# Performance work log

Hardware: AMD Instinct MI355X
Metric: run time of the kernel (lower is better)

The kernel has to match this reference:

```python
import jax, jax.numpy as jnp
import numpy as np

IN, H, B, T = 64, 256, 128, 512

def _uniform(key, shape, std):
    return jax.random.uniform(key, shape, jnp.float32, -std, std)

def setup_inputs() -> dict:
    key = jax.random.key(0)
    ks = jax.random.split(key, 16)
    std = 1.0 / np.sqrt(H)
    inp = {
        'x': jax.random.normal(ks[0], (B, T, IN), jnp.float32),
        # layer 1 sLSTM cell
        'Wxh1': _uniform(ks[1], (4 * H, IN), std), 'bxh1': _uniform(ks[2], (4 * H,), std),
        'Whh1': _uniform(ks[3], (4 * H, H), std),  'bhh1': _uniform(ks[4], (4 * H,), std),
        # layer 2 sLSTM cell
        'Wxh2': _uniform(ks[5], (4 * H, H), std),  'bxh2': _uniform(ks[6], (4 * H,), std),
        'Whh2': _uniform(ks[7], (4 * H, H), std),  'bhh2': _uniform(ks[8], (4 * H,), std),
        # head MLP
        'W1': _uniform(ks[9], (H // 2, H), 1.0 / np.sqrt(H)),      'b1': _uniform(ks[10], (H // 2,), 1.0 / np.sqrt(H)),
        'W2': _uniform(ks[11], (H // 4, H // 2), 1.0 / np.sqrt(H // 2)), 'b2': _uniform(ks[12], (H // 4,), 1.0 / np.sqrt(H // 2)),
        'W3': _uniform(ks[13], (1, H // 4), 1.0 / np.sqrt(H // 4)),      'b3': _uniform(ks[14], (1,), 1.0 / np.sqrt(H // 4)),
    }
    return inp

def _slstm_cell(x, h, c, m, n, Wxh, bxh, Whh, bhh):
    # gates: [B, 4H]
    gates = x @ Wxh.T + bxh + h @ Whh.T + bhh
    ig, fg, zg, og = jnp.split(gates, 4, axis=1)
    z_t = jnp.tanh(zg)
    o_t = jax.nn.sigmoid(og)
    # stabilizer: log(exp(fg)) = fg, log(exp(ig)) = ig
    m_t = jnp.maximum(fg + m, ig)
    i_t = jnp.exp(ig - m_t)
    f_t = jnp.exp(fg + m - m_t)
    c_t = f_t * c + i_t * z_t
    n_t = f_t * n + i_t
    h_t = o_t * (c_t / n_t)
    return h_t, c_t, m_t, n_t

def reference(x, Wxh1, bxh1, Whh1, bhh1, Wxh2, bxh2, Whh2, bhh2, W1, b1, W2, b2, W3, b3):
    Bq = x.shape[0]
    z = jnp.zeros((Bq, H), x.dtype)
    init = (z, z, z, z, z, z, z, z)  # (h1,c1,m1,n1,h2,c2,m2,n2)

    def step(carry, x_t):
        h1, c1, m1, n1, h2, c2, m2, n2 = carry
        h1, c1, m1, n1 = _slstm_cell(x_t, h1, c1, m1, n1, Wxh1, bxh1, Whh1, bhh1)
        h2, c2, m2, n2 = _slstm_cell(h1, h2, c2, m2, n2, Wxh2, bxh2, Whh2, bhh2)
        return (h1, c1, m1, n1, h2, c2, m2, n2), None

    carry, _ = jax.lax.scan(step, init, jnp.swapaxes(x, 0, 1))  # scan over time
    out = carry[4]  # last h2 == outputs[:, -1, :]
    out = jax.nn.relu(out @ W1.T + b1)   # dropout is identity in eval
    out = jax.nn.relu(out @ W2.T + b2)
    out = out @ W3.T + b3
    return out.squeeze(-1)  # [B]
```

## Files before the change

### kernel.cpp

```cpp
#include <hip/hip_runtime.h>
#include <stdint.h>

typedef unsigned short ushort_t;
typedef __attribute__((ext_vector_type(8))) short short8;
typedef __attribute__((ext_vector_type(4))) float float4v;
typedef __attribute__((ext_vector_type(4))) int int4v;

#define TSTEPS 512
#define NBATCH 128
#define HID 256
#define NIN 64
#define RB 32
#define NBHID (NBATCH*HID)
#define RING_DW (RB*NBHID)

#define OFF_FLAGS   0u
#define OFF_BIAS    16384u
#define OFF_H1R     32768u
#define RING_BYTES  (RB*(unsigned)NBATCH*HID*4u)
#define OFF_H2R     (OFF_H1R + RING_BYTES)
#define OFF_WF1     (OFF_H2R + RING_BYTES)
#define WF1_FRAGS   (16*8*4*4)
#define OFF_WF2     (OFF_WF1 + WF1_FRAGS*1024u)
#define WF2_FRAGS   (16*8*6*4)
#define OFF_HOUT    (OFF_WF2 + WF2_FRAGS*1024u)


__device__ __forceinline__ ushort_t bf16h(float f) {
    unsigned u = __float_as_uint(f);
    u += 0x7fffu + ((u >> 16) & 1u);
    return (ushort_t)(u >> 16);
}
__device__ __forceinline__ float bf16f(ushort_t h) {
    return __uint_as_float(((unsigned)h) << 16);
}
__device__ __forceinline__ unsigned genbit(int s) {
    return ((unsigned)(s + 64) >> 5) & 1u;
}


__device__ __forceinline__ int ld_cg_i32(const void* p) {
    int r;
    asm volatile("global_load_dword %0, %1, off sc0 sc1\n\ts_waitcnt vmcnt(0)"
                 : "=v"(r) : "v"(p) : "memory");
    return r;
}
__device__ __forceinline__ float ld_cg_f32(const void* p) {
    float r;
    asm volatile("global_load_dword %0, %1, off sc0 sc1\n\ts_waitcnt vmcnt(0)"
                 : "=v"(r) : "v"(p) : "memory");
    return r;
}
__device__ __forceinline__ void ld2x4(int4v& a, int4v& b, const void* p) {
    asm volatile("global_load_dwordx4 %0, %2, off sc0 sc1\n\t"
                 "global_load_dwordx4 %1, %2, off offset:16 sc0 sc1\n\t"
                 "s_waitcnt vmcnt(0)"
                 : "=&v"(a), "=&v"(b) : "v"(p) : "memory");
}
__device__ __forceinline__ void ld4x4(int4v& a, int4v& b, int4v& c, int4v& d,
                                      const void* p, const void* q) {
    asm volatile("global_load_dwordx4 %0, %4, off sc0 sc1\n\t"
                 "global_load_dwordx4 %1, %4, off offset:16 sc0 sc1\n\t"
                 "global_load_dwordx4 %2, %5, off sc0 sc1\n\t"
                 "global_load_dwordx4 %3, %5, off offset:16 sc0 sc1\n\t"
                 "s_waitcnt vmcnt(0)"
                 : "=&v"(a), "=&v"(b), "=&v"(c), "=&v"(d)
                 : "v"(p), "v"(q) : "memory");
}
__device__ __forceinline__ void st_cg_u32(void* p, unsigned v) {
    asm volatile("global_store_dword %0, %1, off sc0 sc1" :: "v"(p), "v"(v) : "memory");
}
__device__ __forceinline__ void st_cg_i32(int* p, int v) {
    asm volatile("global_store_dword %0, %1, off sc0 sc1" :: "v"(p), "v"(v) : "memory");
}
__device__ __forceinline__ void st_cg_f32(void* p, float v) {
    asm volatile("global_store_dword %0, %1, off sc0 sc1" :: "v"(p), "v"(v) : "memory");
}

__device__ __forceinline__ bool tag8(int4v a, int4v b, unsigned gw) {
    unsigned x = ((unsigned)a[0] ^ gw) | ((unsigned)a[1] ^ gw) |
                 ((unsigned)a[2] ^ gw) | ((unsigned)a[3] ^ gw) |
                 ((unsigned)b[0] ^ gw) | ((unsigned)b[1] ^ gw) |
                 ((unsigned)b[2] ^ gw) | ((unsigned)b[3] ^ gw);
    return (x & 1u) == 0u;
}

__device__ __forceinline__ int4v ext_hi8(int4v a, int4v b) {
    int4v r;
    r[0] = (int)__builtin_amdgcn_perm((unsigned)a[1], (unsigned)a[0], 0x05040100u);
    r[1] = (int)__builtin_amdgcn_perm((unsigned)a[3], (unsigned)a[2], 0x05040100u);
    r[2] = (int)__builtin_amdgcn_perm((unsigned)b[1], (unsigned)b[0], 0x05040100u);
    r[3] = (int)__builtin_amdgcn_perm((unsigned)b[3], (unsigned)b[2], 0x05040100u);
    return r;
}
__device__ __forceinline__ int4v ext_lo8(int4v a, int4v b) {
    int4v r;
    r[0] = (int)__builtin_amdgcn_perm((unsigned)a[1], (unsigned)a[0], 0x07060302u);
    r[1] = (int)__builtin_amdgcn_perm((unsigned)a[3], (unsigned)a[2], 0x07060302u);
    r[2] = (int)__builtin_amdgcn_perm((unsigned)b[1], (unsigned)b[0], 0x07060302u);
    r[3] = (int)__builtin_amdgcn_perm((unsigned)b[3], (unsigned)b[2], 0x07060302u);
    return r;
}


__global__ void prep_misc(const float* bxh1, const float* bhh1,
                          const float* bxh2, const float* bhh2,
                          float* bias, int* flags, unsigned* ring_all)
{
    int n = blockIdx.x * blockDim.x + threadIdx.x;
    if (n < 1024)       bias[n] = bxh1[n] + bhh1[n];
    else if (n < 2048)  bias[n] = bxh2[n - 1024] + bhh2[n - 1024];
    else if (n < 6144)  flags[n - 2048] = 0;
    else {
        unsigned d = n - 6144;
        if (d < 2u * RING_DW)
            ring_all[d] = 0x00000001u;
    }
}

__global__ void prep_wf(const float* Wxh1, const float* Whh1,
                        const float* Wxh2, const float* Whh2,
                        ushort_t* wf1, ushort_t* wf2)
{
    int n = blockIdx.x * blockDim.x + threadIdx.x;
    const int L1E = WF1_FRAGS * 512;
    const int L2E = WF2_FRAGS * 512;
    if (n >= L1E + L2E) return;
    int layer = (n >= L1E) ? 1 : 0;
    int e = layer ? (n - L1E) : n;
    int el = e & 511;
    int f  = e >> 9;
    int lane = el >> 3, j = el & 7;
    int nt = f & 3;
    int rem = f >> 2;
    int i, wv, slice, F, S;
    if (!layer) { F = 4; S = 10; i = rem & 3; wv = (rem >> 2) & 7; slice = rem >> 5; }
    else        { F = 6; S = 16; i = rem % 6; int r2 = rem / 6; wv = r2 & 7; slice = r2 >> 3; }
    int fg = wv * F + i;
    int col = lane & 15;
    int row = nt * 256 + slice * 16 + col;
    float val = 0.f;
    if (fg < 3 * S) {
        int sec = (fg < S) ? 0 : ((fg < 2 * S) ? 1 : 2);
        int ks = (fg - sec * S) * 32 + (lane >> 4) * 8 + j;
        float w;
        if (!layer) w = (ks < 256) ? Whh1[row * 256 + ks] : Wxh1[row * 64 + (ks - 256)];
        else        w = (ks < 256) ? Wxh2[row * 256 + ks] : Whh2[row * 256 + (ks - 256)];
        ushort_t hi = bf16h(w);
        val = (sec < 2) ? bf16f(hi) : (w - bf16f(hi));
    }
    (layer ? wf2 : wf1)[e] = bf16h(val);
}


template<int LAYER, int F, int S, int PITCH>
__device__ __forceinline__ void run_layer(
    int g, int slice, int tid, const float* __restrict__ x,
    int* flags, const float* bias,
    unsigned* h1r, unsigned* h2r, const ushort_t* wfrag, float* hOut,
    ushort_t* sA, ushort_t* sB, float (*red)[4][64][4])
{
    const int wv = tid >> 6, lane = tid & 63;
    const int mrow = lane & 15, q = lane >> 4;
    int* f1 = flags + g * 256;
    int* f2 = flags + 2048 + g * 256;
    int* myflag = flags + LAYER * 2048 + g * 256 + slice * 16;

    short8 bw[4][F];
    {
        const ushort_t* base = wfrag + (size_t)((slice * 8 + wv) * F) * 4 * 512;
        #pragma unroll
        for (int i = 0; i < F; i++)
            #pragma unroll
            for (int nt = 0; nt < 4; nt++)
                bw[nt][i] = *(const short8*)(base + (i * 4 + nt) * 512 + lane * 8);
    }

    float bs[4];
    #pragma unroll
    for (int nt = 0; nt < 4; nt++)
        bs[nt] = bias[LAYER * 1024 + nt * 256 + slice * 16 + mrow];

    float cst[4] = {0,0,0,0}, mst[4] = {0,0,0,0}, nst[4] = {0,0,0,0};

    const int sr = tid >> 5, k = tid & 31;
    const int row = g * 16 + sr;

    for (int t = 0; t < TSTEPS; t++) {
        if (LAYER == 0 && tid >= 128 && tid < 256) {
            int idx = tid - 128;
            int r = idx >> 3, o = idx & 7;
            const float* xsrc = x + ((size_t)(g * 16 + r) * TSTEPS + t) * NIN + o * 8;
            float4v x0 = *(const float4v*)xsrc;
            float4v x1 = *(const float4v*)(xsrc + 4);
            float xs[8] = {x0[0], x0[1], x0[2], x0[3], x1[0], x1[1], x1[2], x1[3]};
            union { ushort_t u[8]; int4v v4; } hiP, loP;
            #pragma unroll
            for (int z = 0; z < 8; z++) {
                ushort_t hi = bf16h(xs[z]);
                hiP.u[z] = hi;
                loP.u[z] = bf16h(xs[z] - bf16f(hi));
            }
            *(int4v*)(sA + r * PITCH + (32 + o) * 8) = hiP.v4;
            *(int4v*)(sB + r * PITCH + (32 + o) * 8) = loP.v4;
        }

        if (tid >= 64 && tid < 128) {
            int pl = tid - 64;
            if (pl < 16) {
                const unsigned* sp;
                unsigned want;
                if (LAYER == 0) {
                    sp = h1r + (size_t)((t - 1) & (RB - 1)) * NBHID
                             + (size_t)(g * 16 + 15) * HID + pl * 16 + 15;
                    want = genbit(t - 1);
                } else {
                    sp = h1r + (size_t)(t & (RB - 1)) * NBHID
                             + (size_t)(g * 16 + 15) * HID + pl * 16 + 15;
                    want = genbit(t);
                }
                while ((((unsigned)ld_cg_i32(sp)) & 1u) != want) { }
            } else if (pl < 32) {
                if (LAYER == 1) {
                    const unsigned* sp = h2r + (size_t)((t - 1) & (RB - 1)) * NBHID
                                             + (size_t)(g * 16 + 15) * HID + (pl - 16) * 16 + 15;
                    unsigned want = genbit(t - 1);
                    while ((((unsigned)ld_cg_i32(sp)) & 1u) != want) { }
                }
            } else if ((t & 7) == 0) {
                int thr = t - 22;
                const int* p = nullptr;
                if (LAYER == 0) {
                    if (pl < 48)      p = f1 + (pl - 32) * 16;
                    else              p = f2 + (pl - 48) * 16;
                } else {
                    if (pl < 48)      p = f2 + (pl - 32) * 16;
                }
                if (p)
                    while (ld_cg_i32(p) < thr) { }
            }
        }
        __syncthreads();

        {
            if (LAYER == 0) {
                const unsigned* base = h1r + ((size_t)((t - 1) & (RB - 1)) * NBATCH + row) * HID + k * 8;
                unsigned w = genbit(t - 1);
                int4v a, b;
                do { ld2x4(a, b, base); } while (!tag8(a, b, w));
                *(int4v*)(sA + sr * PITCH + k * 8) = ext_hi8(a, b);
                *(int4v*)(sB + sr * PITCH + k * 8) = ext_lo8(a, b);
            } else {
                const unsigned* b1 = h1r + ((size_t)(t & (RB - 1)) * NBATCH + row) * HID + k * 8;
                const unsigned* b2 = h2r + ((size_t)((t - 1) & (RB - 1)) * NBATCH + row) * HID + k * 8;
                unsigned w1 = genbit(t), w2 = genbit(t - 1);
                int4v a, b, c, d;
                do { ld4x4(a, b, c, d, b1, b2); } while (!(tag8(a, b, w1) && tag8(c, d, w2)));
                *(int4v*)(sA + sr * PITCH + k * 8)        = ext_hi8(a, b);
                *(int4v*)(sB + sr * PITCH + k * 8)        = ext_lo8(a, b);
                *(int4v*)(sA + sr * PITCH + (32 + k) * 8) = ext_hi8(c, d);
                *(int4v*)(sB + sr * PITCH + (32 + k) * 8) = ext_lo8(c, d);
            }
        }
        __syncthreads();

        if (tid == 256 && (t & 7) == 0)
            st_cg_i32(myflag, t);

        float4v acc[4] = {};
        #pragma unroll
        for (int i = 0; i < F; i++) {
            const int fg = wv * F + i;
            short8 a;
            if (fg < 3 * S) {
                int sec = (fg >= S && fg < 2 * S) ? 1 : 0;
                int ks = ((fg < S) ? fg : ((fg < 2 * S) ? fg - S : fg - 2 * S)) * 32;
                const ushort_t* ap = (sec ? sB : sA) + mrow * PITCH + ks + q * 8;
                a = *(const short8*)ap;
            } else {
                a = (short8){0,0,0,0,0,0,0,0};
            }
            #pragma unroll
            for (int nt = 0; nt < 4; nt++)
                acc[nt] = __builtin_amdgcn_mfma_f32_16x16x32_bf16(a, bw[nt][i], acc[nt], 0, 0, 0);
        }

        if (wv != 0) {
            #pragma unroll
            for (int nt = 0; nt < 4; nt++) *(float4v*)red[wv - 1][nt][lane] = acc[nt];
        }
        __syncthreads();

        if (wv == 0) {
            #pragma unroll
            for (int w = 0; w < 7; w++)
                #pragma unroll
                for (int nt = 0; nt < 4; nt++)
                    acc[nt] += *(const float4v*)red[w][nt][lane];

            unsigned* ring = LAYER ? h2r : h1r;
            unsigned* base = ring + (size_t)(t & (RB - 1)) * NBHID;
            unsigned gw = genbit(t);
            #pragma unroll
            for (int r2 = 0; r2 < 4; r2++) {
                float ig  = acc[0][r2] + bs[0];
                float fgt = acc[1][r2] + bs[1];
                float zg  = acc[2][r2] + bs[2];
                float og  = acc[3][r2] + bs[3];
                float zc = fminf(fmaxf(zg, -15.f), 15.f);
                float e2 = __expf(2.f * zc);
                float zt = (e2 - 1.f) / (e2 + 1.f);
                float ot = 1.f / (1.f + __expf(-og));
                float mt = fmaxf(fgt + mst[r2], ig);
                float it = __expf(ig - mt);
                float ft = __expf(fgt + mst[r2] - mt);
                cst[r2] = ft * cst[r2] + it * zt;
                nst[r2] = ft * nst[r2] + it;
                mst[r2] = mt;
                float h = ot * (cst[r2] / nst[r2]);
                ushort_t hi = (ushort_t)(((unsigned)bf16h(h) & 0xFFFEu) | gw);
                float rem = h - bf16f(hi);
                ushort_t lo = bf16h(rem);
                int orow = g * 16 + q * 4 + r2;
                int col = slice * 16 + mrow;
                st_cg_u32(base + (size_t)orow * HID + col, ((unsigned)lo << 16) | (unsigned)hi);
                if (LAYER == 1 && t == TSTEPS - 1)
                    st_cg_f32(hOut + (size_t)orow * HID + col, h);
            }
        }
    }
}

__global__ __launch_bounds__(512, 2) void recur(
    const float* __restrict__ x,
    int* flags, const float* bias,
    unsigned* h1r, unsigned* h2r, const ushort_t* wf1, const ushort_t* wf2, float* hOut)
{
    __shared__ alignas(16) ushort_t sA[16 * 520];
    __shared__ alignas(16) ushort_t sB[16 * 520];
    __shared__ float red[7][4][64][4];
    int g = blockIdx.x & 7;
    int loc = blockIdx.x >> 3;
    if (loc < 16)
        run_layer<0, 4, 10, 328>(g, loc, threadIdx.x, x, flags, bias, h1r, h2r, wf1, hOut, sA, sB, red);
    else
        run_layer<1, 6, 16, 520>(g, loc - 16, threadIdx.x, x, flags, bias, h1r, h2r, wf2, hOut, sA, sB, red);
}


__global__ void head_mlp(const float* hOut, const float* W1, const float* b1,
                         const float* W2, const float* b2, const float* W3, const float* b3,
                         float* out)
{
    __shared__ float h[256];
    __shared__ float a1[128];
    __shared__ float a2[64];
    int b = blockIdx.x, j = threadIdx.x;
    for (int k = j; k < 256; k += 128)
        h[k] = ld_cg_f32(hOut + (size_t)b * HID + k);
    __syncthreads();
    float s = b1[j];
    for (int k = 0; k < 256; k++) s += W1[j * 256 + k] * h[k];
    a1[j] = fmaxf(s, 0.f);
    __syncthreads();
    if (j < 64) {
        float s2 = b2[j];
        for (int k = 0; k < 128; k++) s2 += W2[j * 128 + k] * a1[k];
        a2[j] = fmaxf(s2, 0.f);
    }
    __syncthreads();
    if (j == 0) {
        float s3 = b3[0];
        for (int k = 0; k < 64; k++) s3 += W3[k] * a2[k];
        out[b] = s3;
    }
}


extern "C" void kernel_launch(void* const* d_in, const int* in_sizes, int n_in,
                              void* d_out, int out_size, void* d_ws, size_t ws_size,
                              hipStream_t stream)
{
    const float* x    = (const float*)d_in[0];
    const float* Wxh1 = (const float*)d_in[1];
    const float* bxh1 = (const float*)d_in[2];
    const float* Whh1 = (const float*)d_in[3];
    const float* bhh1 = (const float*)d_in[4];
    const float* Wxh2 = (const float*)d_in[5];
    const float* bxh2 = (const float*)d_in[6];
    const float* Whh2 = (const float*)d_in[7];
    const float* bhh2 = (const float*)d_in[8];
    const float* W1   = (const float*)d_in[9];
    const float* b1   = (const float*)d_in[10];
    const float* W2   = (const float*)d_in[11];
    const float* b2   = (const float*)d_in[12];
    const float* W3   = (const float*)d_in[13];
    const float* b3   = (const float*)d_in[14];

    char* w = (char*)d_ws;
    int*      flags = (int*)(w + OFF_FLAGS);
    float*    bias  = (float*)(w + OFF_BIAS);
    unsigned* h1r   = (unsigned*)(w + OFF_H1R);
    unsigned* h2r   = (unsigned*)(w + OFF_H2R);
    ushort_t* wf1   = (ushort_t*)(w + OFF_WF1);
    ushort_t* wf2   = (ushort_t*)(w + OFF_WF2);
    float*    hOut  = (float*)(w + OFF_HOUT);

    prep_misc<<<(6144 + 2 * RING_DW + 255) / 256, 256, 0, stream>>>(
        bxh1, bhh1, bxh2, bhh2, bias, flags, h1r);
    prep_wf<<<((WF1_FRAGS + WF2_FRAGS) * 512 + 255) / 256, 256, 0, stream>>>(
        Wxh1, Whh1, Wxh2, Whh2, wf1, wf2);

    const float* xp = x;
    void* args[] = { (void*)&xp, (void*)&flags, (void*)&bias,
                     (void*)&h1r, (void*)&h2r, (void*)&wf1, (void*)&wf2, (void*)&hOut };
    hipLaunchCooperativeKernel((void*)recur, dim3(256), dim3(512), args, 0, stream);

    head_mlp<<<NBATCH, 128, 0, stream>>>(hOut, W1, b1, W2, b2, W3, b3, (float*)d_out);
}
```

Measured before the change: 1.863 ms.

## Add fast-path rings with narrower cache scope and fallback to system-coherent ring

Duplicates each hidden-state ring into a second buffer that is written and polled with sc0-only (narrower-scope) loads and stores, while still writing the system-scope ring. Consumers first spin a bounded number of times on the fast ring and, if the tag never matches, drop into a per-block slow mode that uses the fully coherent ring. The goal is lower cross-CU handoff latency per timestep. In exchange every output is stored twice, prep clears twice as much memory, and on MI355X's multi-XCD layout the sc0 path may never become visible across dies, so the bounded retries can add delay before falling back.

```diff
diff --git a/kernel.cpp b/kernel.cpp
--- a/kernel.cpp
+++ b/kernel.cpp
@@ -19,7 +19,9 @@
 #define OFF_H1R     32768u
 #define RING_BYTES  (RB*(unsigned)NBATCH*HID*4u)
 #define OFF_H2R     (OFF_H1R + RING_BYTES)
-#define OFF_WF1     (OFF_H2R + RING_BYTES)
+#define OFF_H1F     (OFF_H2R + RING_BYTES)
+#define OFF_H2F     (OFF_H1F + RING_BYTES)
+#define OFF_WF1     (OFF_H2F + RING_BYTES)
 #define WF1_FRAGS   (16*8*4*4)
 #define OFF_WF2     (OFF_WF1 + WF1_FRAGS*1024u)
 #define WF2_FRAGS   (16*8*6*4)
@@ -39,10 +41,15 @@
 }
 
 
-__device__ __forceinline__ int ld_cg_i32(const void* p) {
+template<bool SYS>
+__device__ __forceinline__ int ld_i32(const void* p) {
     int r;
-    asm volatile("global_load_dword %0, %1, off sc0 sc1\n\ts_waitcnt vmcnt(0)"
-                 : "=v"(r) : "v"(p) : "memory");
+    if constexpr (SYS)
+        asm volatile("global_load_dword %0, %1, off sc0 sc1\n\ts_waitcnt vmcnt(0)"
+                     : "=v"(r) : "v"(p) : "memory");
+    else
+        asm volatile("global_load_dword %0, %1, off sc0\n\ts_waitcnt vmcnt(0)"
+                     : "=v"(r) : "v"(p) : "memory");
     return r;
 }
 __device__ __forceinline__ float ld_cg_f32(const void* p) {
@@ -51,23 +58,43 @@
                  : "=v"(r) : "v"(p) : "memory");
     return r;
 }
+template<bool SYS>
 __device__ __forceinline__ void ld2x4(int4v& a, int4v& b, const void* p) {
-    asm volatile("global_load_dwordx4 %0, %2, off sc0 sc1\n\t"
-                 "global_load_dwordx4 %1, %2, off offset:16 sc0 sc1\n\t"
-                 "s_waitcnt vmcnt(0)"
-                 : "=&v"(a), "=&v"(b) : "v"(p) : "memory");
-}
+    if constexpr (SYS)
+        asm volatile("global_load_dwordx4 %0, %2, off sc0 sc1\n\t"
+                     "global_load_dwordx4 %1, %2, off offset:16 sc0 sc1\n\t"
+                     "s_waitcnt vmcnt(0)"
+                     : "=&v"(a), "=&v"(b) : "v"(p) : "memory");
+    else
+        asm volatile("global_load_dwordx4 %0, %2, off sc0\n\t"
+                     "global_load_dwordx4 %1, %2, off offset:16 sc0\n\t"
+                     "s_waitcnt vmcnt(0)"
+                     : "=&v"(a), "=&v"(b) : "v"(p) : "memory");
+}
+template<bool SYS>
 __device__ __forceinline__ void ld4x4(int4v& a, int4v& b, int4v& c, int4v& d,
                                       const void* p, const void* q) {
-    asm volatile("global_load_dwordx4 %0, %4, off sc0 sc1\n\t"
-                 "global_load_dwordx4 %1, %4, off offset:16 sc0 sc1\n\t"
-                 "global_load_dwordx4 %2, %5, off sc0 sc1\n\t"
-                 "global_load_dwordx4 %3, %5, off offset:16 sc0 sc1\n\t"
-                 "s_waitcnt vmcnt(0)"
-                 : "=&v"(a), "=&v"(b), "=&v"(c), "=&v"(d)
-                 : "v"(p), "v"(q) : "memory");
-}
-__device__ __forceinline__ void st_cg_u32(void* p, unsigned v) {
+    if constexpr (SYS)
+        asm volatile("global_load_dwordx4 %0, %4, off sc0 sc1\n\t"
+                     "global_load_dwordx4 %1, %4, off offset:16 sc0 sc1\n\t"
+                     "global_load_dwordx4 %2, %5, off sc0 sc1\n\t"
+                     "global_load_dwordx4 %3, %5, off offset:16 sc0 sc1\n\t"
+                     "s_waitcnt vmcnt(0)"
+                     : "=&v"(a), "=&v"(b), "=&v"(c), "=&v"(d)
+                     : "v"(p), "v"(q) : "memory");
+    else
+        asm volatile("global_load_dwordx4 %0, %4, off sc0\n\t"
+                     "global_load_dwordx4 %1, %4, off offset:16 sc0\n\t"
+                     "global_load_dwordx4 %2, %5, off sc0\n\t"
+                     "global_load_dwordx4 %3, %5, off offset:16 sc0\n\t"
+                     "s_waitcnt vmcnt(0)"
+                     : "=&v"(a), "=&v"(b), "=&v"(c), "=&v"(d)
+                     : "v"(p), "v"(q) : "memory");
+}
+__device__ __forceinline__ void st_u32_fast(void* p, unsigned v) {
+    asm volatile("global_store_dword %0, %1, off sc0" :: "v"(p), "v"(v) : "memory");
+}
+__device__ __forceinline__ void st_u32_safe(void* p, unsigned v) {
     asm volatile("global_store_dword %0, %1, off sc0 sc1" :: "v"(p), "v"(v) : "memory");
 }
 __device__ __forceinline__ void st_cg_i32(int* p, int v) {
@@ -113,7 +140,7 @@
     else if (n < 6144)  flags[n - 2048] = 0;
     else {
         unsigned d = n - 6144;
-        if (d < 2u * RING_DW)
+        if (d < 4u * RING_DW)
             ring_all[d] = 0x00000001u;
     }
 }
@@ -157,8 +184,9 @@
 __device__ __forceinline__ void run_layer(
     int g, int slice, int tid, const float* __restrict__ x,
     int* flags, const float* bias,
-    unsigned* h1r, unsigned* h2r, const ushort_t* wfrag, float* hOut,
-    ushort_t* sA, ushort_t* sB, float (*red)[4][64][4])
+    unsigned* h1r, unsigned* h2r, unsigned* h1f, unsigned* h2f,
+    const ushort_t* wfrag, float* hOut,
+    ushort_t* sA, ushort_t* sB, float (*red)[4][64][4], int* fastMode)
 {
     const int wv = tid >> 6, lane = tid & 63;
     const int mrow = lane & 15, q = lane >> 4;
@@ -185,6 +213,9 @@
 
     const int sr = tid >> 5, k = tid & 31;
     const int row = g * 16 + sr;
+
+    if (tid == 0) *fastMode = 1;
+    __syncthreads();
 
     for (int t = 0; t < TSTEPS; t++) {
         if (LAYER == 0 && tid >= 128 && tid < 256) {
@@ -207,27 +238,39 @@
 
         if (tid >= 64 && tid < 128) {
             int pl = tid - 64;
-            if (pl < 16) {
-                const unsigned* sp;
-                unsigned want;
-                if (LAYER == 0) {
-                    sp = h1r + (size_t)((t - 1) & (RB - 1)) * NBHID
-                             + (size_t)(g * 16 + 15) * HID + pl * 16 + 15;
-                    want = genbit(t - 1);
+            const unsigned *spF = nullptr, *spS = nullptr;
+            unsigned want = 0;
+            if (LAYER == 0) {
+                if (pl < 16) {
+                    size_t off = (size_t)((t - 1) & (RB - 1)) * NBHID
+                               + (size_t)(g * 16 + 15) * HID + pl * 16 + 15;
+                    spF = h1f + off; spS = h1r + off; want = genbit(t - 1);
+                }
+            } else {
+                if (pl < 16) {
+                    size_t off = (size_t)(t & (RB - 1)) * NBHID
+                               + (size_t)(g * 16 + 15) * HID + pl * 16 + 15;
+                    spF = h1f + off; spS = h1r + off; want = genbit(t);
+                } else if (pl < 32) {
+                    size_t off = (size_t)((t - 1) & (RB - 1)) * NBHID
+                               + (size_t)(g * 16 + 15) * HID + (pl - 16) * 16 + 15;
+                    spF = h2f + off; spS = h2r + off; want = genbit(t - 1);
+                }
+            }
+            if (spF) {
+                if (*fastMode) {
+                    bool ok = false;
+                    for (int it = 0; it < 256; it++) {
+                        if ((((unsigned)ld_i32<false>(spF)) & 1u) == want) { ok = true; break; }
+                    }
+                    if (!ok) {
+                        *fastMode = 0;
+                        while ((((unsigned)ld_i32<true>(spS)) & 1u) != want) { }
+                    }
                 } else {
-                    sp = h1r + (size_t)(t & (RB - 1)) * NBHID
-                             + (size_t)(g * 16 + 15) * HID + pl * 16 + 15;
-                    want = genbit(t);
-                }
-                while ((((unsigned)ld_cg_i32(sp)) & 1u) != want) { }
-            } else if (pl < 32) {
-                if (LAYER == 1) {
-                    const unsigned* sp = h2r + (size_t)((t - 1) & (RB - 1)) * NBHID
-                                             + (size_t)(g * 16 + 15) * HID + (pl - 16) * 16 + 15;
-                    unsigned want = genbit(t - 1);
-                    while ((((unsigned)ld_cg_i32(sp)) & 1u) != want) { }
-                }
-            } else if ((t & 7) == 0) {
+                    while ((((unsigned)ld_i32<true>(spS)) & 1u) != want) { }
+                }
+            } else if (pl >= 32 && (t & 7) == 0) {
                 int thr = t - 22;
                 const int* p = nullptr;
                 if (LAYER == 0) {
@@ -237,25 +280,47 @@
                     if (pl < 48)      p = f2 + (pl - 32) * 16;
                 }
                 if (p)
-                    while (ld_cg_i32(p) < thr) { }
+                    while (ld_i32<true>(p) < thr) { }
             }
         }
         __syncthreads();
 
         {
+            const bool fm = (*fastMode != 0);
             if (LAYER == 0) {
-                const unsigned* base = h1r + ((size_t)((t - 1) & (RB - 1)) * NBATCH + row) * HID + k * 8;
+                size_t off = ((size_t)((t - 1) & (RB - 1)) * NBATCH + row) * HID + k * 8;
                 unsigned w = genbit(t - 1);
                 int4v a, b;
-                do { ld2x4(a, b, base); } while (!tag8(a, b, w));
+                bool ok = false;
+                if (fm) {
+                    for (int it = 0; it < 32; it++) {
+                        ld2x4<false>(a, b, h1f + off);
+                        if (tag8(a, b, w)) { ok = true; break; }
+                    }
+                }
+                if (!ok) {
+                    if (fm) *fastMode = 0;
+                    do { ld2x4<true>(a, b, h1r + off); } while (!tag8(a, b, w));
+                }
                 *(int4v*)(sA + sr * PITCH + k * 8) = ext_hi8(a, b);
                 *(int4v*)(sB + sr * PITCH + k * 8) = ext_lo8(a, b);
             } else {
-                const unsigned* b1 = h1r + ((size_t)(t & (RB - 1)) * NBATCH + row) * HID + k * 8;
-                const unsigned* b2 = h2r + ((size_t)((t - 1) & (RB - 1)) * NBATCH + row) * HID + k * 8;
+                size_t off1 = ((size_t)(t & (RB - 1)) * NBATCH + row) * HID + k * 8;
+                size_t off2 = ((size_t)((t - 1) & (RB - 1)) * NBATCH + row) * HID + k * 8;
                 unsigned w1 = genbit(t), w2 = genbit(t - 1);
                 int4v a, b, c, d;
-                do { ld4x4(a, b, c, d, b1, b2); } while (!(tag8(a, b, w1) && tag8(c, d, w2)));
+                bool ok = false;
+                if (fm) {
+                    for (int it = 0; it < 32; it++) {
+                        ld4x4<false>(a, b, c, d, h1f + off1, h2f + off2);
+                        if (tag8(a, b, w1) && tag8(c, d, w2)) { ok = true; break; }
+                    }
+                }
+                if (!ok) {
+                    if (fm) *fastMode = 0;
+                    do { ld4x4<true>(a, b, c, d, h1r + off1, h2r + off2); }
+                    while (!(tag8(a, b, w1) && tag8(c, d, w2)));
+                }
                 *(int4v*)(sA + sr * PITCH + k * 8)        = ext_hi8(a, b);
                 *(int4v*)(sB + sr * PITCH + k * 8)        = ext_lo8(a, b);
                 *(int4v*)(sA + sr * PITCH + (32 + k) * 8) = ext_hi8(c, d);
@@ -298,8 +363,8 @@
                 for (int nt = 0; nt < 4; nt++)
                     acc[nt] += *(const float4v*)red[w][nt][lane];
 
-            unsigned* ring = LAYER ? h2r : h1r;
-            unsigned* base = ring + (size_t)(t & (RB - 1)) * NBHID;
+            unsigned* baseS = (LAYER ? h2r : h1r) + (size_t)(t & (RB - 1)) * NBHID;
+            unsigned* baseF = (LAYER ? h2f : h1f) + (size_t)(t & (RB - 1)) * NBHID;
             unsigned gw = genbit(t);
             #pragma unroll
             for (int r2 = 0; r2 < 4; r2++) {
@@ -321,11 +386,14 @@
                 ushort_t hi = (ushort_t)(((unsigned)bf16h(h) & 0xFFFEu) | gw);
                 float rem = h - bf16f(hi);
                 ushort_t lo = bf16h(rem);
+                unsigned word = ((unsigned)lo << 16) | (unsigned)hi;
                 int orow = g * 16 + q * 4 + r2;
                 int col = slice * 16 + mrow;
-                st_cg_u32(base + (size_t)orow * HID + col, ((unsigned)lo << 16) | (unsigned)hi);
+                size_t idx = (size_t)orow * HID + col;
+                st_u32_fast(baseF + idx, word);
+                st_u32_safe(baseS + idx, word);
                 if (LAYER == 1 && t == TSTEPS - 1)
-                    st_cg_f32(hOut + (size_t)orow * HID + col, h);
+                    st_cg_f32(hOut + idx, h);
             }
         }
     }
@@ -334,17 +402,21 @@
 __global__ __launch_bounds__(512, 2) void recur(
     const float* __restrict__ x,
     int* flags, const float* bias,
-    unsigned* h1r, unsigned* h2r, const ushort_t* wf1, const ushort_t* wf2, float* hOut)
+    unsigned* h1r, unsigned* h2r, unsigned* h1f, unsigned* h2f,
+    const ushort_t* wf1, const ushort_t* wf2, float* hOut)
 {
     __shared__ alignas(16) ushort_t sA[16 * 520];
     __shared__ alignas(16) ushort_t sB[16 * 520];
     __shared__ float red[7][4][64][4];
+    __shared__ int fastMode;
     int g = blockIdx.x & 7;
     int loc = blockIdx.x >> 3;
     if (loc < 16)
-        run_layer<0, 4, 10, 328>(g, loc, threadIdx.x, x, flags, bias, h1r, h2r, wf1, hOut, sA, sB, red);
+        run_layer<0, 4, 10, 328>(g, loc, threadIdx.x, x, flags, bias,
+                                 h1r, h2r, h1f, h2f, wf1, hOut, sA, sB, red, &fastMode);
     else
-        run_layer<1, 6, 16, 520>(g, loc - 16, threadIdx.x, x, flags, bias, h1r, h2r, wf2, hOut, sA, sB, red);
+        run_layer<1, 6, 16, 520>(g, loc - 16, threadIdx.x, x, flags, bias,
+                                 h1r, h2r, h1f, h2f, wf2, hOut, sA, sB, red, &fastMode);
 }
 
 
@@ -402,18 +474,21 @@
     float*    bias  = (float*)(w + OFF_BIAS);
     unsigned* h1r   = (unsigned*)(w + OFF_H1R);
     unsigned* h2r   = (unsigned*)(w + OFF_H2R);
+    unsigned* h1f   = (unsigned*)(w + OFF_H1F);
+    unsigned* h2f   = (unsigned*)(w + OFF_H2F);
     ushort_t* wf1   = (ushort_t*)(w + OFF_WF1);
     ushort_t* wf2   = (ushort_t*)(w + OFF_WF2);
     float*    hOut  = (float*)(w + OFF_HOUT);
 
-    prep_misc<<<(6144 + 2 * RING_DW + 255) / 256, 256, 0, stream>>>(
+    prep_misc<<<(6144 + 4 * RING_DW + 255) / 256, 256, 0, stream>>>(
         bxh1, bhh1, bxh2, bhh2, bias, flags, h1r);
     prep_wf<<<((WF1_FRAGS + WF2_FRAGS) * 512 + 255) / 256, 256, 0, stream>>>(
         Wxh1, Whh1, Wxh2, Whh2, wf1, wf2);
 
     const float* xp = x;
     void* args[] = { (void*)&xp, (void*)&flags, (void*)&bias,
-                     (void*)&h1r, (void*)&h2r, (void*)&wf1, (void*)&wf2, (void*)&hOut };
+                     (void*)&h1r, (void*)&h2r, (void*)&h1f, (void*)&h2f,
+                     (void*)&wf1, (void*)&wf2, (void*)&hOut };
     hipLaunchCooperativeKernel((void*)recur, dim3(256), dim3(512), args, 0, stream);
 
     head_mlp<<<NBATCH, 128, 0, stream>>>(hOut, W1, b1, W2, b2, W3, b3, (float*)d_out);
```

Result: slower. 1.912 ms (+2.7%).
